# Kernel tuning notes

Hardware: AMD Instinct MI355X
Metric: run time of the kernel (lower is better)

## Reference

```python
import jax, jax.numpy as jnp
import numpy as np


def setup_inputs() -> dict:
    key = jax.random.key(0)
    k1, k2 = jax.random.split(key)
    shape = (16384, 2048)
    pred_Y = jax.random.uniform(k1, shape, dtype=jnp.float32)
    # gt is a divisor; keep it positive and bounded away from zero-ish via uniform(0,1)
    gt_Y = jax.random.uniform(k2, shape, dtype=jnp.float32)
    return {"pred_Y": pred_Y, "gt_Y": gt_Y}


def reference(pred_Y, gt_Y):
    # NAE: sum over all elements of |pred - gt| / gt, divided by n_sample.
    # Faithful to the original's nested-loop accumulation, expressed as one
    # fused abs-sub-div-sum reduction.
    n_sample = gt_Y.shape[0]
    return jnp.sum(jnp.abs(pred_Y - gt_Y) / gt_Y) / n_sample
```

## Files before the change

### kernel.cpp

```cpp
#include <hip/hip_runtime.h>


#define NAE_BLOCKS  2048
#define NAE_THREADS 256

__global__ __launch_bounds__(NAE_THREADS) void nae_partial_kernel(
    const float* __restrict__ pred,
    const float* __restrict__ gt,
    double* __restrict__ partial,
    long long n4,
    long long n)
{
    const float4* __restrict__ p4 = reinterpret_cast<const float4*>(pred);
    const float4* __restrict__ g4 = reinterpret_cast<const float4*>(gt);

    long long tid    = (long long)blockIdx.x * blockDim.x + threadIdx.x;
    long long stride = (long long)gridDim.x * blockDim.x;

    double acc = 0.0;
    for (long long i = tid; i < n4; i += stride) {
        float4 p = p4[i];
        float4 g = g4[i];
        float tx = (g.x != 0.0f) ? (fabsf(p.x - g.x) / g.x) : 0.0f;
        float ty = (g.y != 0.0f) ? (fabsf(p.y - g.y) / g.y) : 0.0f;
        float tz = (g.z != 0.0f) ? (fabsf(p.z - g.z) / g.z) : 0.0f;
        float tw = (g.w != 0.0f) ? (fabsf(p.w - g.w) / g.w) : 0.0f;
        acc += (double)tx + (double)ty + (double)tz + (double)tw;
    }

    if (blockIdx.x == 0 && threadIdx.x == 0) {
        for (long long i = n4 * 4; i < n; ++i) {
            float g = gt[i];
            if (g != 0.0f) acc += (double)(fabsf(pred[i] - g) / g);
        }
    }

    #pragma unroll
    for (int off = 32; off > 0; off >>= 1)
        acc += __shfl_down(acc, off, 64);

    __shared__ double smem[NAE_THREADS / 64];
    int lane = threadIdx.x & 63;
    int wave = threadIdx.x >> 6;
    if (lane == 0) smem[wave] = acc;
    __syncthreads();

    if (threadIdx.x == 0) {
        double s = 0.0;
        #pragma unroll
        for (int w = 0; w < NAE_THREADS / 64; ++w) s += smem[w];
        partial[blockIdx.x] = s;
    }
}

__global__ __launch_bounds__(NAE_THREADS) void nae_final_kernel(
    const double* __restrict__ partial,
    float* __restrict__ out,
    int nblocks,
    double inv_n)
{
    double acc = 0.0;
    for (int i = threadIdx.x; i < nblocks; i += blockDim.x)
        acc += partial[i];

    #pragma unroll
    for (int off = 32; off > 0; off >>= 1)
        acc += __shfl_down(acc, off, 64);

    __shared__ double smem[NAE_THREADS / 64];
    int lane = threadIdx.x & 63;
    int wave = threadIdx.x >> 6;
    if (lane == 0) smem[wave] = acc;
    __syncthreads();

    if (threadIdx.x == 0) {
        double s = 0.0;
        #pragma unroll
        for (int w = 0; w < NAE_THREADS / 64; ++w) s += smem[w];
        out[0] = (float)(s * inv_n);
    }
}

extern "C" void kernel_launch(void* const* d_in, const int* in_sizes, int n_in,
                              void* d_out, int out_size, void* d_ws, size_t ws_size,
                              hipStream_t stream)
{
    const float* pred = (const float*)d_in[0];
    const float* gt   = (const float*)d_in[1];
    float* out        = (float*)d_out;
    double* partial   = (double*)d_ws;

    long long n  = (long long)in_sizes[0];
    long long n4 = n / 4;

    double inv_n = 1.0 / 16384.0;

    nae_partial_kernel<<<NAE_BLOCKS, NAE_THREADS, 0, stream>>>(pred, gt, partial, n4, n);
    nae_final_kernel<<<1, NAE_THREADS, 0, stream>>>(partial, out, NAE_BLOCKS, inv_n);
}
```

Before: 47.90 us.

## Fuse final reduction via last-block atomic counter and specialize fixed-size load loop

Merges the two-kernel reduction into one kernel where the last block to finish, found with an atomic counter, sums the per-block partials. Adds a fast path for the exact input size that uses a fixed 16-iteration int-indexed loop, and accumulates each float4 in fp32 before converting to double, which reduces fp64 adds. Drops the second kernel launch but adds a memset and threadfences, and slightly changes accumulation precision.

New measurement: 104.0 us. 117% more time.

```diff
diff --git a/kernel.cpp b/kernel.cpp
--- a/kernel.cpp
+++ b/kernel.cpp
@@ -1,37 +1,52 @@
 #include <hip/hip_runtime.h>
 
 
-#define NAE_BLOCKS  2048
-#define NAE_THREADS 256
+#define NAE_BLOCKS       2048
+#define NAE_THREADS      256
+#define F4_PER_THREAD    16
 
-__global__ __launch_bounds__(NAE_THREADS) void nae_partial_kernel(
+__device__ __forceinline__ float nae_term4_f32(float4 p, float4 g) {
+    float tx = (g.x != 0.0f) ? (fabsf(p.x - g.x) / g.x) : 0.0f;
+    float ty = (g.y != 0.0f) ? (fabsf(p.y - g.y) / g.y) : 0.0f;
+    float tz = (g.z != 0.0f) ? (fabsf(p.z - g.z) / g.z) : 0.0f;
+    float tw = (g.w != 0.0f) ? (fabsf(p.w - g.w) / g.w) : 0.0f;
+    return (tx + ty) + (tz + tw);
+}
+
+__global__ __launch_bounds__(NAE_THREADS) void nae_fused_kernel(
     const float* __restrict__ pred,
     const float* __restrict__ gt,
     double* __restrict__ partial,
+    unsigned int* __restrict__ counter,
+    float* __restrict__ out,
     long long n4,
-    long long n)
+    long long n,
+    double inv_n)
 {
     const float4* __restrict__ p4 = reinterpret_cast<const float4*>(pred);
     const float4* __restrict__ g4 = reinterpret_cast<const float4*>(gt);
 
-    long long tid    = (long long)blockIdx.x * blockDim.x + threadIdx.x;
-    long long stride = (long long)gridDim.x * blockDim.x;
+    double acc = 0.0;
 
-    double acc = 0.0;
-    for (long long i = tid; i < n4; i += stride) {
-        float4 p = p4[i];
-        float4 g = g4[i];
-        float tx = (g.x != 0.0f) ? (fabsf(p.x - g.x) / g.x) : 0.0f;
-        float ty = (g.y != 0.0f) ? (fabsf(p.y - g.y) / g.y) : 0.0f;
-        float tz = (g.z != 0.0f) ? (fabsf(p.z - g.z) / g.z) : 0.0f;
-        float tw = (g.w != 0.0f) ? (fabsf(p.w - g.w) / g.w) : 0.0f;
-        acc += (double)tx + (double)ty + (double)tz + (double)tw;
-    }
-
-    if (blockIdx.x == 0 && threadIdx.x == 0) {
-        for (long long i = n4 * 4; i < n; ++i) {
-            float g = gt[i];
-            if (g != 0.0f) acc += (double)(fabsf(pred[i] - g) / g);
+    if (n4 == (long long)NAE_BLOCKS * NAE_THREADS * F4_PER_THREAD &&
+        gridDim.x == NAE_BLOCKS) {
+        int base = (int)blockIdx.x * (NAE_THREADS * F4_PER_THREAD) + (int)threadIdx.x;
+        for (int k = 0; k < F4_PER_THREAD; ++k) {
+            int i = base + k * NAE_THREADS;
+            float4 p = p4[i];
+            float4 g = g4[i];
+            acc += (double)nae_term4_f32(p, g);
+        }
+    } else {
+        long long tid = (long long)blockIdx.x * blockDim.x + threadIdx.x;
+        long long tpg = (long long)gridDim.x * blockDim.x;
+        for (long long i = tid; i < n4; i += tpg)
+            acc += (double)nae_term4_f32(p4[i], g4[i]);
+        if (blockIdx.x == 0 && threadIdx.x == 0) {
+            for (long long i = n4 * 4; i < n; ++i) {
+                float g = gt[i];
+                if (g != 0.0f) acc += (double)(fabsf(pred[i] - g) / g);
+            }
         }
     }
 
@@ -40,6 +55,7 @@
         acc += __shfl_down(acc, off, 64);
 
     __shared__ double smem[NAE_THREADS / 64];
+    __shared__ bool is_last;
     int lane = threadIdx.x & 63;
     int wave = threadIdx.x >> 6;
     if (lane == 0) smem[wave] = acc;
@@ -50,34 +66,28 @@
         #pragma unroll
         for (int w = 0; w < NAE_THREADS / 64; ++w) s += smem[w];
         partial[blockIdx.x] = s;
+        __threadfence();
+        unsigned int v = atomicAdd(counter, 1u);
+        is_last = (v == gridDim.x - 1);
     }
-}
-
-__global__ __launch_bounds__(NAE_THREADS) void nae_final_kernel(
-    const double* __restrict__ partial,
-    float* __restrict__ out,
-    int nblocks,
-    double inv_n)
-{
-    double acc = 0.0;
-    for (int i = threadIdx.x; i < nblocks; i += blockDim.x)
-        acc += partial[i];
-
-    #pragma unroll
-    for (int off = 32; off > 0; off >>= 1)
-        acc += __shfl_down(acc, off, 64);
-
-    __shared__ double smem[NAE_THREADS / 64];
-    int lane = threadIdx.x & 63;
-    int wave = threadIdx.x >> 6;
-    if (lane == 0) smem[wave] = acc;
     __syncthreads();
 
-    if (threadIdx.x == 0) {
-        double s = 0.0;
+    if (is_last) {
+        __threadfence();
+        double a = 0.0;
+        for (unsigned int i = threadIdx.x; i < gridDim.x; i += blockDim.x)
+            a += partial[i];
         #pragma unroll
-        for (int w = 0; w < NAE_THREADS / 64; ++w) s += smem[w];
-        out[0] = (float)(s * inv_n);
+        for (int off = 32; off > 0; off >>= 1)
+            a += __shfl_down(a, off, 64);
+        if (lane == 0) smem[wave] = a;
+        __syncthreads();
+        if (threadIdx.x == 0) {
+            double s = 0.0;
+            #pragma unroll
+            for (int w = 0; w < NAE_THREADS / 64; ++w) s += smem[w];
+            out[0] = (float)(s * inv_n);
+        }
     }
 }
 
@@ -88,13 +98,16 @@
     const float* pred = (const float*)d_in[0];
     const float* gt   = (const float*)d_in[1];
     float* out        = (float*)d_out;
-    double* partial   = (double*)d_ws;
+
+    unsigned int* counter = (unsigned int*)d_ws;
+    double* partial       = (double*)((char*)d_ws + 512);
 
     long long n  = (long long)in_sizes[0];
     long long n4 = n / 4;
 
     double inv_n = 1.0 / 16384.0;
 
-    nae_partial_kernel<<<NAE_BLOCKS, NAE_THREADS, 0, stream>>>(pred, gt, partial, n4, n);
-    nae_final_kernel<<<1, NAE_THREADS, 0, stream>>>(partial, out, NAE_BLOCKS, inv_n);
+    hipMemsetAsync(counter, 0, sizeof(unsigned int), stream);
+    nae_fused_kernel<<<NAE_BLOCKS, NAE_THREADS, 0, stream>>>(
+        pred, gt, partial, counter, out, n4, n, inv_n);
 }
```
